# Optimization experiments

Measured on AMD Instinct MI355X. Metric: run time of the kernel, lower is better.

## Reference

```python
import jax, jax.numpy as jnp
import numpy as np


def _quat_to_rot(q):
    # q: [B,4] (w,x,y,z); normalize as the torch code does when norm != 1
    q = q / jnp.linalg.norm(q, axis=-1, keepdims=True)
    w, x, y, z = q[:, 0], q[:, 1], q[:, 2], q[:, 3]
    r00 = 1 - 2 * y**2 - 2 * z**2
    r01 = 2 * x * y - 2 * z * w
    r02 = 2 * x * z + 2 * y * w
    r10 = 2 * x * y + 2 * z * w
    r11 = 1 - 2 * x**2 - 2 * z**2
    r12 = 2 * y * z - 2 * x * w
    r20 = 2 * x * z - 2 * y * w
    r21 = 2 * y * z + 2 * x * w
    r22 = 1 - 2 * x**2 - 2 * y**2
    R = jnp.stack([
        jnp.stack([r00, r01, r02], axis=-1),
        jnp.stack([r10, r11, r12], axis=-1),
        jnp.stack([r20, r21, r22], axis=-1),
    ], axis=-2)  # [B,3,3]
    return R


def setup_inputs() -> dict:
    key = jax.random.key(0)
    k1, k2, k3, k4 = jax.random.split(key, 4)
    B, N = 32, 262144
    return {
        "pcd_mis": jax.random.normal(k1, (B, N, 3), dtype=jnp.float32),
        "T_mis": jax.random.normal(k2, (B, 4, 4), dtype=jnp.float32),
        "delta_q_pred": jax.random.normal(k3, (B, 4), dtype=jnp.float32),
        "delta_t_pred": jax.random.normal(k4, (B, 3), dtype=jnp.float32),
    }


def reference(pcd_mis, T_mis, delta_q_pred, delta_t_pred):
    B = delta_q_pred.shape[0]
    R = _quat_to_rot(delta_q_pred)                      # [B,3,3]
    t = delta_t_pred[:, :, None]                        # [B,3,1]
    top = jnp.concatenate([R, t], axis=-1)              # [B,3,4]
    bottom = jnp.broadcast_to(
        jnp.array([0.0, 0.0, 0.0, 1.0], dtype=pcd_mis.dtype), (B, 1, 4))
    delta_T = jnp.concatenate([top, bottom], axis=-2)   # [B,4,4]
    inv_T = jnp.linalg.inv(delta_T)                     # [B,4,4]
    batch_T_pred = jnp.einsum('bij,bjk->bik', inv_T, T_mis)  # [B,4,4]
    # homogeneous point transform: only first 3 output rows are kept
    # new = (inv_T @ [p;1])[:3] = p @ Rinv^T + tinv
    pcd_new = jnp.einsum('bij,bnj->bni', inv_T[:, :3, :3], pcd_mis) \
        + inv_T[:, None, :3, 3]                          # [B,N,3]
    return (batch_T_pred, pcd_new)
```

## Files before the change

### kernel.cpp

```cpp
#include <hip/hip_runtime.h>
#include <math.h>

struct Inv {
    float i00, i01, i02, it0;
    float i10, i11, i12, it1;
    float i20, i21, i22, it2;
};

__device__ __forceinline__ Inv make_inv(const float* __restrict__ q,
                                        const float* __restrict__ t, int b) {
    float w = q[b * 4 + 0], x = q[b * 4 + 1], y = q[b * 4 + 2], z = q[b * 4 + 3];
    float inv_n = 1.0f / sqrtf(w * w + x * x + y * y + z * z);
    w *= inv_n; x *= inv_n; y *= inv_n; z *= inv_n;
    float R00 = 1.f - 2.f * y * y - 2.f * z * z;
    float R01 = 2.f * x * y - 2.f * z * w;
    float R02 = 2.f * x * z + 2.f * y * w;
    float R10 = 2.f * x * y + 2.f * z * w;
    float R11 = 1.f - 2.f * x * x - 2.f * z * z;
    float R12 = 2.f * y * z - 2.f * x * w;
    float R20 = 2.f * x * z - 2.f * y * w;
    float R21 = 2.f * y * z + 2.f * x * w;
    float R22 = 1.f - 2.f * x * x - 2.f * y * y;
    float t0 = t[b * 3 + 0], t1 = t[b * 3 + 1], t2 = t[b * 3 + 2];
    Inv v;
    v.i00 = R00; v.i01 = R10; v.i02 = R20; v.it0 = -(R00 * t0 + R10 * t1 + R20 * t2);
    v.i10 = R01; v.i11 = R11; v.i12 = R21; v.it1 = -(R01 * t0 + R11 * t1 + R21 * t2);
    v.i20 = R02; v.i21 = R12; v.i22 = R22; v.it2 = -(R02 * t0 + R12 * t1 + R22 * t2);
    return v;
}

__device__ __forceinline__ void xf(const Inv& M, float px, float py, float pz,
                                   float& ox, float& oy, float& oz) {
    ox = fmaf(M.i00, px, fmaf(M.i01, py, fmaf(M.i02, pz, M.it0)));
    oy = fmaf(M.i10, px, fmaf(M.i11, py, fmaf(M.i12, pz, M.it1)));
    oz = fmaf(M.i20, px, fmaf(M.i21, py, fmaf(M.i22, pz, M.it2)));
}

using nat_f4 = __attribute__((ext_vector_type(4))) float;
__device__ __forceinline__ void store_nt(float4* p, const float4& v) {
    __builtin_nontemporal_store(*(const nat_f4*)&v, (nat_f4*)p);
}

__global__ __launch_bounds__(256) void realign_stream_kernel(
        const float4* __restrict__ pcd,
        const float* __restrict__ T_mis,
        const float* __restrict__ q,
        const float* __restrict__ t,
        float* __restrict__ out_mat,
        float4* __restrict__ out_pcd,
        int f4_per_batch) {
    const int b = blockIdx.y;
    const int tid = threadIdx.x;

    const size_t base = (size_t)b * (size_t)f4_per_batch
                      + (size_t)blockIdx.x * 768u + (size_t)tid * 3u;

    const float4 v0 = pcd[base + 0];
    const float4 v1 = pcd[base + 1];
    const float4 v2 = pcd[base + 2];

    const Inv M = make_inv(q, t, b);

    if (blockIdx.x == 0 && tid < 16) {
        const int i = tid >> 2;
        const int j = tid & 3;
        const float* Tb = T_mis + b * 16;
        float val;
        if (i < 3) {
            float a0, a1, a2, it;
            if (i == 0)      { a0 = M.i00; a1 = M.i01; a2 = M.i02; it = M.it0; }
            else if (i == 1) { a0 = M.i10; a1 = M.i11; a2 = M.i12; it = M.it1; }
            else             { a0 = M.i20; a1 = M.i21; a2 = M.i22; it = M.it2; }
            val = fmaf(a0, Tb[0 * 4 + j],
                  fmaf(a1, Tb[1 * 4 + j],
                  fmaf(a2, Tb[2 * 4 + j],
                       it * Tb[3 * 4 + j])));
        } else {
            val = Tb[3 * 4 + j];
        }
        out_mat[b * 16 + tid] = val;
    }

    float4 o0, o1, o2;
    xf(M, v0.x, v0.y, v0.z, o0.x, o0.y, o0.z);
    xf(M, v0.w, v1.x, v1.y, o0.w, o1.x, o1.y);
    xf(M, v1.z, v1.w, v2.x, o1.z, o1.w, o2.x);
    xf(M, v2.y, v2.z, v2.w, o2.y, o2.z, o2.w);

    store_nt(&out_pcd[base + 0], o0);
    store_nt(&out_pcd[base + 1], o1);
    store_nt(&out_pcd[base + 2], o2);
}

extern "C" void kernel_launch(void* const* d_in, const int* in_sizes, int n_in,
                              void* d_out, int out_size, void* d_ws, size_t ws_size,
                              hipStream_t stream) {
    const float* pcd   = (const float*)d_in[0];
    const float* T_mis = (const float*)d_in[1];
    const float* q     = (const float*)d_in[2];
    const float* t     = (const float*)d_in[3];
    float* out = (float*)d_out;

    const int B = in_sizes[2] / 4;
    const long long N = (long long)in_sizes[0] / (3LL * B);
    const int f4_per_batch = (int)(3 * N / 4);
    const int blocks_x = f4_per_batch / 768;

    dim3 grid(blocks_x, B);
    realign_stream_kernel<<<grid, 256, 0, stream>>>(
        (const float4*)pcd, T_mis, q, t,
        out, (float4*)(out + B * 16), f4_per_batch);
}
```

Baseline: 194.4 us.

## Use one float4 per thread with cross-lane shuffles for point-phase alignment

Each thread now loads and stores a single contiguous float4, so every wavefront access is fully coalesced. This replaces the old stride-3 float4 pattern, where each thread handled three float4s. Neighbouring components needed to complete a point are fetched with wave shuffles, and boundary lanes fall back to scalar global loads. The grid becomes 1D with three times as many threads, and the batch index comes from a readfirstlane division. Stores switch from nontemporal to ordinary and loads become nontemporal. Costs include phase-based divergence (w%3), extra scalar boundary loads, and three times as many blocks, each recomputing the inverse matrix.

Result: faster. 180.0 us (-7.4%).

```diff
diff --git a/kernel.cpp b/kernel.cpp
--- a/kernel.cpp
+++ b/kernel.cpp
@@ -37,59 +37,81 @@
 }
 
 using nat_f4 = __attribute__((ext_vector_type(4))) float;
-__device__ __forceinline__ void store_nt(float4* p, const float4& v) {
-    __builtin_nontemporal_store(*(const nat_f4*)&v, (nat_f4*)p);
+__device__ __forceinline__ float4 load_nt(const float4* p) {
+    nat_f4 v = __builtin_nontemporal_load((const nat_f4*)p);
+    float4 r; *(nat_f4*)&r = v; return r;
 }
 
-__global__ __launch_bounds__(256) void realign_stream_kernel(
+__global__ __launch_bounds__(256) void realign_phase_kernel(
         const float4* __restrict__ pcd,
         const float* __restrict__ T_mis,
         const float* __restrict__ q,
         const float* __restrict__ t,
         float* __restrict__ out_mat,
         float4* __restrict__ out_pcd,
-        int f4_per_batch) {
-    const int b = blockIdx.y;
-    const int tid = threadIdx.x;
+        int f4_per_batch, int total_f4) {
+    const int w    = blockIdx.x * 256 + threadIdx.x;
+    const int lane = threadIdx.x & 63;
 
-    const size_t base = (size_t)b * (size_t)f4_per_batch
-                      + (size_t)blockIdx.x * 768u + (size_t)tid * 3u;
+    const float4 A = load_nt(&pcd[w]);
 
-    const float4 v0 = pcd[base + 0];
-    const float4 v1 = pcd[base + 1];
-    const float4 v2 = pcd[base + 2];
+    float lom2 = __shfl_up(A.z, 1);
+    float lom1 = __shfl_up(A.w, 1);
+    float hi4  = __shfl_down(A.x, 1);
+    float hi5  = __shfl_down(A.y, 1);
 
-    const Inv M = make_inv(q, t, b);
+    const float* pf = (const float*)pcd;
+    if (lane == 0 && w > 0) {
+        lom2 = pf[4 * w - 2];
+        lom1 = pf[4 * w - 1];
+    }
+    if (lane == 63 && w + 1 < total_f4) {
+        hi4 = pf[4 * w + 4];
+        hi5 = pf[4 * w + 5];
+    }
 
-    if (blockIdx.x == 0 && tid < 16) {
-        const int i = tid >> 2;
-        const int j = tid & 3;
-        const float* Tb = T_mis + b * 16;
+    const int wb = __builtin_amdgcn_readfirstlane(w);
+    const int b  = wb / f4_per_batch;
+    const Inv M  = make_inv(q, t, b);
+
+    if (w < 512) {
+        const int bb = w >> 4;
+        const int i  = (w >> 2) & 3;
+        const int j  = w & 3;
+        const Inv Mb = make_inv(q, t, bb);
+        const float* Tb = T_mis + bb * 16;
         float val;
         if (i < 3) {
-            float a0, a1, a2, it;
-            if (i == 0)      { a0 = M.i00; a1 = M.i01; a2 = M.i02; it = M.it0; }
-            else if (i == 1) { a0 = M.i10; a1 = M.i11; a2 = M.i12; it = M.it1; }
-            else             { a0 = M.i20; a1 = M.i21; a2 = M.i22; it = M.it2; }
+            float a0, a1, a2, itr;
+            if (i == 0)      { a0 = Mb.i00; a1 = Mb.i01; a2 = Mb.i02; itr = Mb.it0; }
+            else if (i == 1) { a0 = Mb.i10; a1 = Mb.i11; a2 = Mb.i12; itr = Mb.it1; }
+            else             { a0 = Mb.i20; a1 = Mb.i21; a2 = Mb.i22; itr = Mb.it2; }
             val = fmaf(a0, Tb[0 * 4 + j],
                   fmaf(a1, Tb[1 * 4 + j],
                   fmaf(a2, Tb[2 * 4 + j],
-                       it * Tb[3 * 4 + j])));
+                       itr * Tb[3 * 4 + j])));
         } else {
             val = Tb[3 * 4 + j];
         }
-        out_mat[b * 16 + tid] = val;
+        out_mat[w] = val;
     }
 
-    float4 o0, o1, o2;
-    xf(M, v0.x, v0.y, v0.z, o0.x, o0.y, o0.z);
-    xf(M, v0.w, v1.x, v1.y, o0.w, o1.x, o1.y);
-    xf(M, v1.z, v1.w, v2.x, o1.z, o1.w, o2.x);
-    xf(M, v2.y, v2.z, v2.w, o2.y, o2.z, o2.w);
+    const int phi = w % 3;
+    float4 o;
+    if (phi == 0) {
+        xf(M, A.x, A.y, A.z, o.x, o.y, o.z);
+        o.w = fmaf(M.i00, A.w, fmaf(M.i01, hi4, fmaf(M.i02, hi5, M.it0)));
+    } else if (phi == 1) {
+        o.x = fmaf(M.i10, lom1, fmaf(M.i11, A.x, fmaf(M.i12, A.y, M.it1)));
+        o.y = fmaf(M.i20, lom1, fmaf(M.i21, A.x, fmaf(M.i22, A.y, M.it2)));
+        o.z = fmaf(M.i00, A.z,  fmaf(M.i01, A.w, fmaf(M.i02, hi4, M.it0)));
+        o.w = fmaf(M.i10, A.z,  fmaf(M.i11, A.w, fmaf(M.i12, hi4, M.it1)));
+    } else {
+        o.x = fmaf(M.i20, lom2, fmaf(M.i21, lom1, fmaf(M.i22, A.x, M.it2)));
+        xf(M, A.y, A.z, A.w, o.y, o.z, o.w);
+    }
 
-    store_nt(&out_pcd[base + 0], o0);
-    store_nt(&out_pcd[base + 1], o1);
-    store_nt(&out_pcd[base + 2], o2);
+    out_pcd[w] = o;
 }
 
 extern "C" void kernel_launch(void* const* d_in, const int* in_sizes, int n_in,
@@ -104,10 +126,10 @@
     const int B = in_sizes[2] / 4;
     const long long N = (long long)in_sizes[0] / (3LL * B);
     const int f4_per_batch = (int)(3 * N / 4);
-    const int blocks_x = f4_per_batch / 768;
+    const int total_f4 = f4_per_batch * B;
+    const int blocks = total_f4 / 256;
 
-    dim3 grid(blocks_x, B);
-    realign_stream_kernel<<<grid, 256, 0, stream>>>(
+    realign_phase_kernel<<<dim3(blocks), 256, 0, stream>>>(
         (const float4*)pcd, T_mis, q, t,
-        out, (float4*)(out + B * 16), f4_per_batch);
+        out, (float4*)(out + B * 16), f4_per_batch, total_f4);
 }
```
